# Kernel optimization log

Measured on AMD Instinct MI355X. Metric: run time of the kernel, lower is better.

## Reference

```python
import jax, jax.numpy as jnp
import numpy as np

EMBED = 1024
HEADS = 16
HEAD_DIM = EMBED // HEADS


def setup_inputs() -> dict:
    key = jax.random.key(0)
    ks = jax.random.split(key, 6)
    B, S, E = 2, 2048, EMBED
    x = jax.random.normal(ks[0], (B, S, E), dtype=jnp.float32)
    # torch nn.Linear stores weight as [out, in]; scale ~ 1/sqrt(E) like default init
    sc = 1.0 / np.sqrt(E)
    Wq = jax.random.normal(ks[1], (E, E), dtype=jnp.float32) * sc
    Wk = jax.random.normal(ks[2], (E, E), dtype=jnp.float32) * sc
    Wv = jax.random.normal(ks[3], (E, E), dtype=jnp.float32) * sc
    Wo = jax.random.normal(ks[4], (E, E), dtype=jnp.float32) * sc
    bo = jnp.zeros((E,), dtype=jnp.float32)
    # causal mask, broadcastable [1,1,S,S]; mask==0 positions get -inf
    mask = jnp.tril(jnp.ones((S, S), dtype=jnp.int32))[None, None]
    return {"x": x, "mask": mask, "Wq": Wq, "Wk": Wk, "Wv": Wv, "Wo": Wo, "bo": bo}


def reference(x, mask, Wq, Wk, Wv, Wo, bo):
    B, S, E = x.shape
    # Linear(x) = x @ W.T (torch convention, no bias)
    Q = (x @ Wq.T).reshape(B, S, HEADS, HEAD_DIM).transpose(0, 2, 1, 3)  # [B,H,S,D]
    K = (x @ Wk.T).reshape(B, S, HEADS, HEAD_DIM).transpose(0, 2, 1, 3)
    V = (x @ Wv.T).reshape(B, S, HEADS, HEAD_DIM).transpose(0, 2, 1, 3)
    scale = 1.0 / jnp.sqrt(jnp.float32(HEAD_DIM))
    scores = jnp.einsum("bhqd,bhkd->bhqk", Q, K) * scale  # [B,H,S,S]
    scores = jnp.where(mask == 0, -jnp.inf, scores)
    attn = jax.nn.softmax(scores, axis=-1)
    out = jnp.einsum("bhqk,bhkd->bhqd", attn, V)  # [B,H,S,D]
    out = out.transpose(0, 2, 1, 3).reshape(B, S, E)
    return out @ Wo.T + bo
```

## Files before the change

kernel.cpp:

```cpp
#include <hip/hip_runtime.h>
#include <hip/hip_bf16.h>

typedef unsigned short u16;
typedef unsigned int u32;

#define B_ 2
#define S_ 2048
#define E_ 1024
#define H_ 16
#define D_ 64

typedef __bf16 bf16_8 __attribute__((ext_vector_type(8)));
typedef __bf16 bf16_4 __attribute__((ext_vector_type(4)));
typedef float f32_4 __attribute__((ext_vector_type(4)));

typedef const __attribute__((address_space(1))) void* gptr_t;
typedef __attribute__((address_space(3))) void* sptr_t;

__device__ __forceinline__ void gload_lds16(const void* g, void* l) {
  __builtin_amdgcn_global_load_lds((gptr_t)g, (sptr_t)l, 16, 0, 0);
}

__device__ __forceinline__ u16 f2bf(float f) {
  union { float f; u32 u; } v; v.f = f;
  u32 u = v.u;
  u32 r = (u + 0x7FFFu + ((u >> 16) & 1u)) >> 16;
  return (u16)r;
}

__global__ __launch_bounds__(256) void cvt_all(
    const float* __restrict__ x,
    const float* __restrict__ wq, const float* __restrict__ wk,
    const float* __restrict__ wv, const float* __restrict__ wo,
    u16* __restrict__ dst)
{
  const int XB = (B_ * S_ * E_) / 1024;
  const int WB = (E_ * E_) / 1024;
  int blk = blockIdx.x;
  const float* src;
  size_t dbase;
  if (blk < XB)           { src = x;  dbase = 0;                         }
  else if (blk < XB+WB)   { src = wq; dbase = (size_t)B_*S_*E_;          blk -= XB; }
  else if (blk < XB+2*WB) { src = wk; dbase = (size_t)B_*S_*E_ + E_*E_;  blk -= XB+WB; }
  else if (blk < XB+3*WB) { src = wv; dbase = (size_t)B_*S_*E_ + 2*(size_t)E_*E_; blk -= XB+2*WB; }
  else                    { src = wo; dbase = (size_t)B_*S_*E_ + 3*(size_t)E_*E_; blk -= XB+3*WB; }
  size_t i = ((size_t)blk * 256 + threadIdx.x) * 4;
  float4 v = *(const float4*)(src + i);
  ushort4 o;
  o.x = f2bf(v.x); o.y = f2bf(v.y); o.z = f2bf(v.z); o.w = f2bf(v.w);
  *(ushort4*)(dst + dbase + i) = o;
}

#define TST 136
__global__ __launch_bounds__(256) void qkv_gemm(
    const u16* __restrict__ x,
    const u16* __restrict__ wq, const u16* __restrict__ wk, const u16* __restrict__ wv,
    u16* __restrict__ q_ws, u16* __restrict__ k_ws, u16* __restrict__ v_ws)
{
  const int K = E_;
  __shared__ __attribute__((aligned(16))) u16 SM[16384];
  u16* As = SM;
  u16* Bs = SM + 8192;
  u16* LB = SM;

  int tid = threadIdx.x;
  int wave = tid >> 6, lane = tid & 63;
  int quad = lane >> 4, fcol = lane & 15;
  int row0 = blockIdx.x * 128;
  int nb = blockIdx.y;
  int which = nb >> 3;
  const u16* W = (which == 0) ? wq : ((which == 1) ? wk : wv);
  int col0 = (nb & 7) * 128;
  int wm = wave >> 1, wn = wave & 1;
  int swzb = fcol & 7;

  f32_4 acc[4][4];
#pragma unroll
  for (int i = 0; i < 4; i++)
#pragma unroll
    for (int j = 0; j < 4; j++) acc[i][j] = f32_4{0.f, 0.f, 0.f, 0.f};

  for (int k0 = 0; k0 < K; k0 += 64) {
#pragma unroll
    for (int i = 0; i < 4; i++) {
      int c = i * 256 + tid;
      int r = c >> 3;
      int kcd = (c & 7) ^ (r & 7);
      gload_lds16(x + (size_t)(row0 + r) * K + k0 + kcd * 8, As + (size_t)c * 8);
      gload_lds16(W + (size_t)(col0 + r) * K + k0 + kcd * 8, Bs + (size_t)c * 8);
    }
    __syncthreads();
#pragma unroll
    for (int ks2 = 0; ks2 < 2; ks2++) {
      bf16_8 a[4], b[4];
#pragma unroll
      for (int mt = 0; mt < 4; mt++) {
        int rm = wm * 64 + mt * 16 + fcol;
        a[mt] = *(const bf16_8*)(As + rm * 64 + (((ks2 * 4 + quad) ^ swzb) << 3));
      }
#pragma unroll
      for (int nt = 0; nt < 4; nt++) {
        int rn = wn * 64 + nt * 16 + fcol;
        b[nt] = *(const bf16_8*)(Bs + rn * 64 + (((ks2 * 4 + quad) ^ swzb) << 3));
      }
#pragma unroll
      for (int mt = 0; mt < 4; mt++)
#pragma unroll
        for (int nt = 0; nt < 4; nt++)
          acc[mt][nt] = __builtin_amdgcn_mfma_f32_16x16x32_bf16(a[mt], b[nt], acc[mt][nt], 0, 0, 0);
    }
    __syncthreads();
  }

  if (which != 2) {
    u16* dst = (which == 0) ? q_ws : k_ws;
#pragma unroll
    for (int p = 0; p < 2; p++) {
      if (wm == p) {
#pragma unroll
        for (int mt = 0; mt < 4; mt++)
#pragma unroll
          for (int nt = 0; nt < 4; nt++)
#pragma unroll
            for (int r = 0; r < 4; r++)
              LB[(mt * 16 + quad * 4 + r) * TST + wn * 64 + nt * 16 + fcol] =
                  f2bf(acc[mt][nt][r]);
      }
      __syncthreads();
#pragma unroll
      for (int i = 0; i < 4; i++) {
        int r_loc = i * 16 + (tid >> 4);
        int c8 = (tid & 15) * 8;
        int hh = (col0 + c8) >> 6, d = c8 & (D_ - 1);
        int grow = row0 + p * 64 + r_loc;
        int b = grow >> 11, s = grow & (S_ - 1);
        *(bf16_8*)(dst + (((size_t)b * H_ + hh) * S_ + s) * D_ + d) =
            *(const bf16_8*)(LB + r_loc * TST + c8);
      }
      __syncthreads();
    }
  } else {
    int b = row0 >> 11, s0 = row0 & (S_ - 1);
#pragma unroll
    for (int p = 0; p < 2; p++) {
      if (wn == p) {
#pragma unroll
        for (int mt = 0; mt < 4; mt++)
#pragma unroll
          for (int nt = 0; nt < 4; nt++)
#pragma unroll
            for (int r = 0; r < 4; r++)
              LB[(nt * 16 + fcol) * TST + wm * 64 + mt * 16 + quad * 4 + r] =
                  f2bf(acc[mt][nt][r]);
      }
      __syncthreads();
      {
        int fl = tid >> 2, tq = tid & 3;
        int F = col0 + p * 64 + fl;
        int h = F >> 6, d = F & (D_ - 1);
        u16* vp = v_ws + (((size_t)b * H_ + h) * D_ + d) * S_ + s0 + tq * 32;
#pragma unroll
        for (int i = 0; i < 4; i++)
          *(bf16_8*)(vp + i * 8) = *(const bf16_8*)(LB + fl * TST + tq * 32 + i * 8);
      }
      __syncthreads();
    }
  }
}

#define AST 72
#define PST 68
__global__ __launch_bounds__(256, 4) void attn_kernel(
    const u16* __restrict__ Qg_, const u16* __restrict__ Kg_,
    const u16* __restrict__ Vg_, u16* __restrict__ Og_)
{
  __shared__ __attribute__((aligned(16))) u16 Ks[64 * AST];
  __shared__ __attribute__((aligned(16))) u16 Vs[64 * AST];
  __shared__ __attribute__((aligned(16))) u16 Ps[4 * 16 * PST];

  int tid = threadIdx.x, wave = tid >> 6, lane = tid & 63;
  int quad = lane >> 4, fcol = lane & 15;
  int blk = blockIdx.x;
  int bh = blk & 31;
  int k = 31 - (blk >> 5);
  int b = bh >> 4, h = bh & (H_ - 1);

  const u16* Qg = Qg_ + (size_t)bh * S_ * D_;
  const u16* Kg = Kg_ + (size_t)bh * S_ * D_;
  const u16* Vg = Vg_ + (size_t)bh * D_ * S_;

  int qb = k * 64 + wave * 16;

  bf16_8 aq[2];
#pragma unroll
  for (int ks2 = 0; ks2 < 2; ks2++)
    aq[ks2] = *(const bf16_8*)(Qg + (size_t)(qb + fcol) * D_ + ks2 * 32 + quad * 8);

  const __bf16 one = (__bf16)1.0f;
  const bf16_8 vone = {one, one, one, one, one, one, one, one};

  f32_4 accO[4];
  f32_4 accL = f32_4{0.f, 0.f, 0.f, 0.f};
#pragma unroll
  for (int nt = 0; nt < 4; nt++) accO[nt] = f32_4{0.f, 0.f, 0.f, 0.f};

  u16* Pw = Ps + wave * 16 * PST;

  for (int j = 0; j <= k; j++) {
#pragma unroll
    for (int i = 0; i < 2; i++) {
      int c = i * 256 + tid;
      int r = c >> 3, cc = (c & 7) * 8;
      *(bf16_8*)(Ks + r * AST + cc) =
          *(const bf16_8*)(Kg + (size_t)(j * 64 + r) * D_ + cc);
      *(bf16_8*)(Vs + r * AST + cc) =
          *(const bf16_8*)(Vg + (size_t)r * S_ + j * 64 + cc);
    }
    __syncthreads();

    f32_4 sc[4];
#pragma unroll
    for (int nt = 0; nt < 4; nt++) sc[nt] = f32_4{0.f, 0.f, 0.f, 0.f};
#pragma unroll
    for (int ks2 = 0; ks2 < 2; ks2++) {
#pragma unroll
      for (int nt = 0; nt < 4; nt++) {
        bf16_8 bk = *(const bf16_8*)(Ks + (nt * 16 + fcol) * AST + ks2 * 32 + quad * 8);
        sc[nt] = __builtin_amdgcn_mfma_f32_16x16x32_bf16(aq[ks2], bk, sc[nt], 0, 0, 0);
      }
    }

    bool partial = (j == k);
    int qrow0 = qb + quad * 4;
    float p[4][4];
#pragma unroll
    for (int nt = 0; nt < 4; nt++) {
      int kv = j * 64 + nt * 16 + fcol;
#pragma unroll
      for (int r = 0; r < 4; r++) {
        float e = __expf(fmaf(sc[nt][r], 0.125f, -12.0f));
        p[nt][r] = (!partial || kv <= qrow0 + r) ? e : 0.f;
      }
    }

#pragma unroll
    for (int nt = 0; nt < 4; nt++)
#pragma unroll
      for (int r = 0; r < 4; r++)
        Pw[(quad * 4 + r) * PST + nt * 16 + fcol] = f2bf(p[nt][r]);

#pragma unroll
    for (int ks2 = 0; ks2 < 2; ks2++) {
      const u16* ab = Pw + fcol * PST + ks2 * 32 + quad * 8;
      bf16_4 lo = *(const bf16_4*)(ab);
      bf16_4 hi = *(const bf16_4*)(ab + 4);
      bf16_8 ap = __builtin_shufflevector(lo, hi, 0, 1, 2, 3, 4, 5, 6, 7);
      accL = __builtin_amdgcn_mfma_f32_16x16x32_bf16(ap, vone, accL, 0, 0, 0);
#pragma unroll
      for (int nt = 0; nt < 4; nt++) {
        bf16_8 bv = *(const bf16_8*)(Vs + (nt * 16 + fcol) * AST + ks2 * 32 + quad * 8);
        accO[nt] = __builtin_amdgcn_mfma_f32_16x16x32_bf16(ap, bv, accO[nt], 0, 0, 0);
      }
    }
    __syncthreads();
  }

#pragma unroll
  for (int r = 0; r < 4; r++) {
    float inv = 1.0f / accL[r];
    int qrow = qb + quad * 4 + r;
#pragma unroll
    for (int nt = 0; nt < 4; nt++) {
      int d = nt * 16 + fcol;
      Og_[((size_t)b * S_ + qrow) * E_ + h * D_ + d] = f2bf(accO[nt][r] * inv);
    }
  }
}

__global__ __launch_bounds__(256) void out_gemm(
    const u16* __restrict__ A, const u16* __restrict__ W,
    const float* __restrict__ bias, float* __restrict__ out)
{
  const int K = E_;
  __shared__ __attribute__((aligned(16))) u16 As[128 * 64];
  __shared__ __attribute__((aligned(16))) u16 Bs[64 * 64];

  int tid = threadIdx.x;
  int wave = tid >> 6, lane = tid & 63;
  int quad = lane >> 4, fcol = lane & 15;
  int row0 = blockIdx.x * 128;
  int col0 = blockIdx.y * 64;
  int swzb = fcol & 7;

  f32_4 acc[2][4];
#pragma unroll
  for (int i = 0; i < 2; i++)
#pragma unroll
    for (int j = 0; j < 4; j++) acc[i][j] = f32_4{0.f, 0.f, 0.f, 0.f};

  for (int k0 = 0; k0 < K; k0 += 64) {
#pragma unroll
    for (int i = 0; i < 4; i++) {
      int c = i * 256 + tid;
      int r = c >> 3;
      int kcd = (c & 7) ^ (r & 7);
      gload_lds16(A + (size_t)(row0 + r) * K + k0 + kcd * 8, As + (size_t)c * 8);
    }
#pragma unroll
    for (int i = 0; i < 2; i++) {
      int c = i * 256 + tid;
      int r = c >> 3;
      int kcd = (c & 7) ^ (r & 7);
      gload_lds16(W + (size_t)(col0 + r) * K + k0 + kcd * 8, Bs + (size_t)c * 8);
    }
    __syncthreads();
#pragma unroll
    for (int ks2 = 0; ks2 < 2; ks2++) {
      bf16_8 a[2], b[4];
#pragma unroll
      for (int mt = 0; mt < 2; mt++) {
        int rm = wave * 32 + mt * 16 + fcol;
        a[mt] = *(const bf16_8*)(As + rm * 64 + (((ks2 * 4 + quad) ^ swzb) << 3));
      }
#pragma unroll
      for (int nt = 0; nt < 4; nt++) {
        int rn = nt * 16 + fcol;
        b[nt] = *(const bf16_8*)(Bs + rn * 64 + (((ks2 * 4 + quad) ^ swzb) << 3));
      }
#pragma unroll
      for (int mt = 0; mt < 2; mt++)
#pragma unroll
        for (int nt = 0; nt < 4; nt++)
          acc[mt][nt] = __builtin_amdgcn_mfma_f32_16x16x32_bf16(a[mt], b[nt], acc[mt][nt], 0, 0, 0);
    }
    __syncthreads();
  }

#pragma unroll
  for (int mt = 0; mt < 2; mt++)
#pragma unroll
    for (int nt = 0; nt < 4; nt++) {
      int gcol = col0 + nt * 16 + fcol;
      float bv = bias[gcol];
#pragma unroll
      for (int r = 0; r < 4; r++) {
        int grow = row0 + wave * 32 + mt * 16 + quad * 4 + r;
        out[(size_t)grow * E_ + gcol] = acc[mt][nt][r] + bv;
      }
    }
}

extern "C" void kernel_launch(void* const* d_in, const int* in_sizes, int n_in,
                              void* d_out, int out_size, void* d_ws, size_t ws_size,
                              hipStream_t stream) {
  const float* x  = (const float*)d_in[0];
  const float* wq = (const float*)d_in[2];
  const float* wk = (const float*)d_in[3];
  const float* wv = (const float*)d_in[4];
  const float* wo = (const float*)d_in[5];
  const float* bo = (const float*)d_in[6];
  float* out = (float*)d_out;

  const size_t sz  = (size_t)B_ * S_ * E_;
  const size_t wsz = (size_t)E_ * E_;
  if (ws_size < (5 * sz + 4 * wsz) * sizeof(u16)) return;

  u16* x_bf  = (u16*)d_ws;
  u16* wq_bf = x_bf + sz;
  u16* wk_bf = wq_bf + wsz;
  u16* wv_bf = wk_bf + wsz;
  u16* wo_bf = wv_bf + wsz;
  u16* q_ws  = wo_bf + wsz;
  u16* k_ws  = q_ws + sz;
  u16* v_ws  = k_ws + sz;
  u16* o_ws  = v_ws + sz;

  cvt_all<<<(int)((sz + 4 * wsz) / 1024), 256, 0, stream>>>(x, wq, wk, wv, wo, x_bf);
  qkv_gemm<<<dim3(32, 24), 256, 0, stream>>>(x_bf, wq_bf, wk_bf, wv_bf, q_ws, k_ws, v_ws);
  attn_kernel<<<dim3(1024), 256, 0, stream>>>(q_ws, k_ws, v_ws, o_ws);
  out_gemm<<<dim3(32, 16), 256, 0, stream>>>(o_ws, wo_bf, bo, out);
}
```

Baseline: 194.1 us.

## Rewrite QKV GEMM as 256x256-tile double-buffered pipeline with interleaved prefetch

Replaces the 128x128 single-buffered QKV GEMM with 256x256 tiles across 8 waves, double-buffered LDS, and global-to-LDS prefetch of the next k-tile interleaved between four MFMA phases. It uses raw s_barrier, vmcnt waits and setprio to overlap memory with compute, and remaps blocks into a grouped order for L2 reuse. The epilogue uses per-wave swizzled LDS scratch to write head-major Q/K and transposed V. Uses 128KB of LDS and only 192 blocks, which limits occupancy and makes correctness depend on hand-placed waits.

```diff
diff --git a/kernel.cpp b/kernel.cpp
--- a/kernel.cpp
+++ b/kernel.cpp
@@ -51,119 +51,191 @@
   *(ushort4*)(dst + dbase + i) = o;
 }
 
-#define TST 136
-__global__ __launch_bounds__(256) void qkv_gemm(
+#define MFMA16 __builtin_amdgcn_mfma_f32_16x16x32_bf16
+#define BARX() asm volatile("s_barrier" ::: "memory")
+
+__global__ __launch_bounds__(512, 2) void qkv_gemm(
     const u16* __restrict__ x,
     const u16* __restrict__ wq, const u16* __restrict__ wk, const u16* __restrict__ wv,
     u16* __restrict__ q_ws, u16* __restrict__ k_ws, u16* __restrict__ v_ws)
 {
   const int K = E_;
-  __shared__ __attribute__((aligned(16))) u16 SM[16384];
-  u16* As = SM;
-  u16* Bs = SM + 8192;
-  u16* LB = SM;
+  __shared__ __attribute__((aligned(16))) u16 SM[65536];
 
   int tid = threadIdx.x;
   int wave = tid >> 6, lane = tid & 63;
   int quad = lane >> 4, fcol = lane & 15;
-  int row0 = blockIdx.x * 128;
-  int nb = blockIdx.y;
-  int which = nb >> 3;
+  int wr = wave >> 2, wc = wave & 3;
+  int swzb = fcol & 7;
+
+  int my = ((blockIdx.x & 7) * 24) + (blockIdx.x >> 3);
+  int rb = my / 12, cb = my % 12;
+  int row0 = rb << 8;
+  int which = cb >> 2;
   const u16* W = (which == 0) ? wq : ((which == 1) ? wk : wv);
-  int col0 = (nb & 7) * 128;
-  int wm = wave >> 1, wn = wave & 1;
-  int swzb = fcol & 7;
-
-  f32_4 acc[4][4];
-#pragma unroll
-  for (int i = 0; i < 4; i++)
-#pragma unroll
-    for (int j = 0; j < 4; j++) acc[i][j] = f32_4{0.f, 0.f, 0.f, 0.f};
-
-  for (int k0 = 0; k0 < K; k0 += 64) {
-#pragma unroll
-    for (int i = 0; i < 4; i++) {
-      int c = i * 256 + tid;
+  int col0 = (cb & 3) << 8;
+
+  auto stg = [&](const u16* src, int srow0, int buf, int bofs, int h, int k0) {
+#pragma unroll
+    for (int i = 0; i < 2; i++) {
+      int c = (i << 9) + tid;
       int r = c >> 3;
       int kcd = (c & 7) ^ (r & 7);
-      gload_lds16(x + (size_t)(row0 + r) * K + k0 + kcd * 8, As + (size_t)c * 8);
-      gload_lds16(W + (size_t)(col0 + r) * K + k0 + kcd * 8, Bs + (size_t)c * 8);
-    }
-    __syncthreads();
-#pragma unroll
-    for (int ks2 = 0; ks2 < 2; ks2++) {
-      bf16_8 a[4], b[4];
-#pragma unroll
-      for (int mt = 0; mt < 4; mt++) {
-        int rm = wm * 64 + mt * 16 + fcol;
-        a[mt] = *(const bf16_8*)(As + rm * 64 + (((ks2 * 4 + quad) ^ swzb) << 3));
-      }
-#pragma unroll
-      for (int nt = 0; nt < 4; nt++) {
-        int rn = wn * 64 + nt * 16 + fcol;
-        b[nt] = *(const bf16_8*)(Bs + rn * 64 + (((ks2 * 4 + quad) ^ swzb) << 3));
-      }
+      gload_lds16(src + (size_t)(srow0 + h * 128 + r) * K + k0 + kcd * 8,
+                  SM + buf * 32768 + bofs + ((h << 10) + c) * 8);
+    }
+  };
+
+  f32_4 acc[8][4];
+#pragma unroll
+  for (int i = 0; i < 8; i++)
+#pragma unroll
+    for (int j = 0; j < 4; j++) acc[i][j] = f32_4{0.f, 0.f, 0.f, 0.f};
+
+  stg(W, col0, 0, 16384, 0, 0);
+  stg(x, row0, 0, 0,     0, 0);
+  stg(W, col0, 0, 16384, 1, 0);
+  stg(x, row0, 0, 0,     1, 0);
+  stg(W, col0, 1, 16384, 0, 64);
+  stg(x, row0, 1, 0,     0, 64);
+  asm volatile("s_waitcnt vmcnt(4)" ::: "memory");
+  BARX();
+
+  int arow = wr * 128 + fcol;
+  int brow = wc * 64 + fcol;
+  int xo0 = (quad ^ swzb) << 3;
+  int xo1 = ((4 + quad) ^ swzb) << 3;
+
+  bf16_8 a[2][4], bl[2][2], bh[2][2];
+
+  for (int kt = 0; kt < 16; ++kt) {
+    int bj = kt & 1;
+    const u16* Ab = SM + bj * 32768;
+    const u16* Bb = Ab + 16384;
+
+#pragma unroll
+    for (int mt = 0; mt < 4; mt++) {
+      a[0][mt] = *(const bf16_8*)(Ab + (arow + mt * 16) * 64 + xo0);
+      a[1][mt] = *(const bf16_8*)(Ab + (arow + mt * 16) * 64 + xo1);
+    }
+#pragma unroll
+    for (int nt = 0; nt < 2; nt++) {
+      bl[0][nt] = *(const bf16_8*)(Bb + (brow + nt * 16) * 64 + xo0);
+      bl[1][nt] = *(const bf16_8*)(Bb + (brow + nt * 16) * 64 + xo1);
+    }
+    if (kt + 1 < 16) stg(W, col0, bj ^ 1, 16384, 1, (kt + 1) * 64);
+    BARX();
+    __builtin_amdgcn_s_setprio(1);
+#pragma unroll
+    for (int ks = 0; ks < 2; ks++)
 #pragma unroll
       for (int mt = 0; mt < 4; mt++)
 #pragma unroll
-        for (int nt = 0; nt < 4; nt++)
-          acc[mt][nt] = __builtin_amdgcn_mfma_f32_16x16x32_bf16(a[mt], b[nt], acc[mt][nt], 0, 0, 0);
-    }
-    __syncthreads();
+        for (int nt = 0; nt < 2; nt++)
+          acc[mt][nt] = MFMA16(a[ks][mt], bl[ks][nt], acc[mt][nt], 0, 0, 0);
+    __builtin_amdgcn_s_setprio(0);
+    BARX();
+
+#pragma unroll
+    for (int nt = 0; nt < 2; nt++) {
+      bh[0][nt] = *(const bf16_8*)(Bb + (brow + (nt + 2) * 16) * 64 + xo0);
+      bh[1][nt] = *(const bf16_8*)(Bb + (brow + (nt + 2) * 16) * 64 + xo1);
+    }
+    if (kt + 1 < 16) stg(x, row0, bj ^ 1, 0, 1, (kt + 1) * 64);
+    BARX();
+    __builtin_amdgcn_s_setprio(1);
+#pragma unroll
+    for (int ks = 0; ks < 2; ks++)
+#pragma unroll
+      for (int mt = 0; mt < 4; mt++)
+#pragma unroll
+        for (int nt = 0; nt < 2; nt++)
+          acc[mt][2 + nt] = MFMA16(a[ks][mt], bh[ks][nt], acc[mt][2 + nt], 0, 0, 0);
+    __builtin_amdgcn_s_setprio(0);
+    BARX();
+
+#pragma unroll
+    for (int mt = 0; mt < 4; mt++) {
+      a[0][mt] = *(const bf16_8*)(Ab + (arow + (mt + 4) * 16) * 64 + xo0);
+      a[1][mt] = *(const bf16_8*)(Ab + (arow + (mt + 4) * 16) * 64 + xo1);
+    }
+    if (kt + 2 < 16) stg(W, col0, bj, 16384, 0, (kt + 2) * 64);
+    BARX();
+    __builtin_amdgcn_s_setprio(1);
+#pragma unroll
+    for (int ks = 0; ks < 2; ks++)
+#pragma unroll
+      for (int mt = 0; mt < 4; mt++)
+#pragma unroll
+        for (int nt = 0; nt < 2; nt++)
+          acc[4 + mt][2 + nt] = MFMA16(a[ks][mt], bh[ks][nt], acc[4 + mt][2 + nt], 0, 0, 0);
+    __builtin_amdgcn_s_setprio(0);
+    BARX();
+
+    if (kt + 2 < 16) stg(x, row0, bj, 0, 0, (kt + 2) * 64);
+    if (kt + 2 < 16) {
+      asm volatile("s_waitcnt vmcnt(4)" ::: "memory");
+    } else if (kt + 1 < 16) {
+      asm volatile("s_waitcnt vmcnt(0)" ::: "memory");
+    }
+    BARX();
+    __builtin_amdgcn_s_setprio(1);
+#pragma unroll
+    for (int ks = 0; ks < 2; ks++)
+#pragma unroll
+      for (int mt = 0; mt < 4; mt++)
+#pragma unroll
+        for (int nt = 0; nt < 2; nt++)
+          acc[4 + mt][nt] = MFMA16(a[ks][mt], bl[ks][nt], acc[4 + mt][nt], 0, 0, 0);
+    __builtin_amdgcn_s_setprio(0);
+    BARX();
   }
 
+  u16* scr = SM + wave * 8192;
+  int h = ((cb & 3) << 2) + wc;
+  int grow0 = row0 + wr * 128;
+  int bb = grow0 >> 11, srow0 = grow0 & (S_ - 1);
+
   if (which != 2) {
+#pragma unroll
+    for (int m = 0; m < 8; m++)
+#pragma unroll
+      for (int n = 0; n < 4; n++)
+#pragma unroll
+        for (int r = 0; r < 4; r++) {
+          int s = m * 16 + quad * 4 + r;
+          int d = n * 16 + fcol;
+          scr[s * 64 + (((d >> 3) ^ (s & 7)) << 3) + (d & 7)] = f2bf(acc[m][n][r]);
+        }
+    __syncthreads();
     u16* dst = (which == 0) ? q_ws : k_ws;
-#pragma unroll
-    for (int p = 0; p < 2; p++) {
-      if (wm == p) {
-#pragma unroll
-        for (int mt = 0; mt < 4; mt++)
-#pragma unroll
-          for (int nt = 0; nt < 4; nt++)
-#pragma unroll
-            for (int r = 0; r < 4; r++)
-              LB[(mt * 16 + quad * 4 + r) * TST + wn * 64 + nt * 16 + fcol] =
-                  f2bf(acc[mt][nt][r]);
-      }
-      __syncthreads();
-#pragma unroll
-      for (int i = 0; i < 4; i++) {
-        int r_loc = i * 16 + (tid >> 4);
-        int c8 = (tid & 15) * 8;
-        int hh = (col0 + c8) >> 6, d = c8 & (D_ - 1);
-        int grow = row0 + p * 64 + r_loc;
-        int b = grow >> 11, s = grow & (S_ - 1);
-        *(bf16_8*)(dst + (((size_t)b * H_ + hh) * S_ + s) * D_ + d) =
-            *(const bf16_8*)(LB + r_loc * TST + c8);
-      }
-      __syncthreads();
+    u16* gp = dst + (((size_t)bb * H_ + h) * S_ + srow0) * D_;
+    int lrow = lane >> 3, cc = lane & 7;
+#pragma unroll
+    for (int i = 0; i < 16; i++) {
+      int sl = i * 8 + lrow;
+      *(bf16_8*)(gp + (size_t)sl * D_ + cc * 8) =
+          *(const bf16_8*)(scr + sl * 64 + ((cc ^ (sl & 7)) << 3));
     }
   } else {
-    int b = row0 >> 11, s0 = row0 & (S_ - 1);
-#pragma unroll
-    for (int p = 0; p < 2; p++) {
-      if (wn == p) {
-#pragma unroll
-        for (int mt = 0; mt < 4; mt++)
-#pragma unroll
-          for (int nt = 0; nt < 4; nt++)
-#pragma unroll
-            for (int r = 0; r < 4; r++)
-              LB[(nt * 16 + fcol) * TST + wm * 64 + mt * 16 + quad * 4 + r] =
-                  f2bf(acc[mt][nt][r]);
-      }
-      __syncthreads();
-      {
-        int fl = tid >> 2, tq = tid & 3;
-        int F = col0 + p * 64 + fl;
-        int h = F >> 6, d = F & (D_ - 1);
-        u16* vp = v_ws + (((size_t)b * H_ + h) * D_ + d) * S_ + s0 + tq * 32;
-#pragma unroll
-        for (int i = 0; i < 4; i++)
-          *(bf16_8*)(vp + i * 8) = *(const bf16_8*)(LB + fl * TST + tq * 32 + i * 8);
-      }
-      __syncthreads();
+#pragma unroll
+    for (int m = 0; m < 8; m++)
+#pragma unroll
+      for (int n = 0; n < 4; n++)
+#pragma unroll
+        for (int r = 0; r < 4; r++) {
+          int s = m * 16 + quad * 4 + r;
+          int d = n * 16 + fcol;
+          scr[d * 128 + (((s >> 3) ^ (d & 15)) << 3) + (s & 7)] = f2bf(acc[m][n][r]);
+        }
+    __syncthreads();
+    size_t base2 = (((size_t)bb * H_ + h) * D_) * S_ + srow0;
+    int lrow = lane >> 4, cc = lane & 15;
+#pragma unroll
+    for (int i = 0; i < 16; i++) {
+      int dl = i * 4 + lrow;
+      *(bf16_8*)(v_ws + base2 + (size_t)dl * S_ + cc * 8) =
+          *(const bf16_8*)(scr + dl * 128 + ((cc ^ (dl & 15)) << 3));
     }
   }
 }
@@ -376,7 +448,7 @@
   u16* o_ws  = v_ws + sz;
 
   cvt_all<<<(int)((sz + 4 * wsz) / 1024), 256, 0, stream>>>(x, wq, wk, wv, wo, x_bf);
-  qkv_gemm<<<dim3(32, 24), 256, 0, stream>>>(x_bf, wq_bf, wk_bf, wv_bf, q_ws, k_ws, v_ws);
+  qkv_gemm<<<dim3(192), 512, 0, stream>>>(x_bf, wq_bf, wk_bf, wv_bf, q_ws, k_ws, v_ws);
   attn_kernel<<<dim3(1024), 256, 0, stream>>>(q_ws, k_ws, v_ws, o_ws);
   out_gemm<<<dim3(32, 16), 256, 0, stream>>>(o_ws, wo_bf, bo, out);
 }
```

Result: faster. 184.2 us (-5.1%).
